# Performance work log

Measured on AMD Instinct MI355X. Metric: run time of the kernel, lower is better.

The kernel has to match this reference:

```python
import jax, jax.numpy as jnp
import numpy as np

B, S, L, K, E, V = 2048, 4, 16, 8, 256, 128  # batch, max_steps, tokens/step, landmarks/cell, emb_sz, vocab


def setup_inputs() -> dict:
    key = jax.random.key(0)
    ks = jax.random.split(key, 10)
    std = 1.0 / (E * 9)
    return {
        "gold_table": jax.random.normal(ks[0], (11, E), jnp.float32),
        "map_table": jax.random.normal(ks[1], (V, E), jnp.float32) * 0.01,  # init_std=0.01
        "conv_weight": jax.random.uniform(ks[2], (E, E, 3, 3), jnp.float32, -std, std),
        "action_table": jax.random.normal(ks[3], (4, 32), jnp.float32),
        "action_W": jax.random.normal(ks[4], (9, 32), jnp.float32) * (1.0 / np.sqrt(32.0)),
        "action_b": jnp.zeros((9,), jnp.float32),
        "goldstandard": jax.random.randint(ks[5], (B, S, L), 0, 11),
        "actions": jax.random.randint(ks[6], (B, S - 1), 0, 4),
        "landmarks": jax.random.randint(ks[7], (B, 4, 4, K), 0, V),
        "y": jax.random.randint(ks[8], (B, 2), 0, 4),
    }


def _extract_patches(x):
    # x: [B,E,4,4] -> [B,9,E,16]; 3x3 neighborhoods with zero padding (conv padding=1)
    xp = jnp.pad(x, ((0, 0), (0, 0), (1, 1), (1, 1)))
    shifts = [xp[:, :, dh:dh + 4, dw:dw + 4].reshape(x.shape[0], x.shape[1], 16)
              for dh in range(3) for dw in range(3)]
    return jnp.stack(shifts, axis=1)


def reference(gold_table, map_table, conv_weight, action_table, action_W, action_b,
              goldstandard, actions, landmarks, y):
    Bn = y.shape[0]
    # goldstandard features: per-step embed+sum over tokens, concat over steps -> [B, S*E]
    emb = gold_table[goldstandard].sum(axis=2).reshape(Bn, -1)
    # MapEmbedding2d with padding_idx=0: zero row 0, embed, sum over landmark list
    mt = map_table.at[0].set(0.0)
    l_emb = mt[landmarks].sum(axis=3).transpose(0, 3, 1, 2)  # [B,E,4,4]
    # action-conditioned 3x3 masks, one per action
    action_out = action_table @ action_W.T + action_b  # [4,9]
    masks = jax.nn.softmax(action_out, axis=1)  # [4,9]
    Wr = conv_weight.reshape(E, E, 9)  # [O,I,tap]
    l_embs = [l_emb]
    cur = l_emb
    for j in range(S - 1):
        # per-sample routed mask == dispatch-to-expert conv; fused gather+masked-conv+scatter
        m = masks[actions[:, j]]  # [B,9]
        patches = _extract_patches(cur)  # [B,9,E,16]
        out = jnp.einsum('btip,bt,oit->bop', patches, m, Wr).reshape(Bn, E, 4, 4)
        l_embs.append(out)
        cur = out
    lm = jnp.concatenate(l_embs, axis=1).reshape(Bn, S * E, 16)  # [B, S*E, 16]
    logits = jnp.einsum('bcp,bc->bp', lm, emb)  # bmm(landmarks^T, emb)
    prob = jax.nn.softmax(logits, axis=1)
    y_true = y[:, 0] * 4 + y[:, 1]
    # torch CrossEntropyLoss applied to prob (softmax twice, as in the original)
    logp = jax.nn.log_softmax(prob, axis=1)
    loss = -jnp.take_along_axis(logp, y_true[:, None], axis=1).mean()
    acc = (jnp.argmax(prob, axis=1) == y_true).astype(jnp.float32).mean()
    return loss, acc, prob
```

## Files before the change

kernel.cpp:

```cpp
#include <hip/hip_runtime.h>
#include <hip/hip_bf16.h>

typedef __attribute__((ext_vector_type(4))) float f32x4;
typedef __attribute__((ext_vector_type(8))) short short8;

__device__ __forceinline__ float bf2f(ushort u) {
    union { unsigned int u; float f; } x; x.u = ((unsigned int)u) << 16; return x.f;
}
__device__ __forceinline__ ushort f2bf(float f) {
    union { float f; unsigned int u; } x; x.f = f;
    unsigned int u = x.u;
    unsigned int r = (u + 0x7fffu + ((u >> 16) & 1u)) >> 16;
    return (ushort)r;
}
__device__ __forceinline__ void gload16(const ushort* g, ushort* l) {
    __builtin_amdgcn_global_load_lds(
        (const __attribute__((address_space(1))) unsigned int*)g,
        (__attribute__((address_space(3))) unsigned int*)l, 16, 0, 0);
}

__global__ __launch_bounds__(256) void k_prep(
    const float* __restrict__ conv_w, const float* __restrict__ a_table,
    const float* __restrict__ a_W, const float* __restrict__ a_b,
    const int* __restrict__ actions, int* __restrict__ cnt,
    int* __restrict__ list, ushort* __restrict__ Wa,
    float* __restrict__ out_head)
{
    __shared__ float ao[4][9];
    __shared__ float m[4][9];
    const int bid = blockIdx.x, tid = threadIdx.x;
    if (bid < 256) {
        if (tid < 36) {
            const int a = tid / 9, t = tid % 9;
            float s = a_b[t];
            for (int c = 0; c < 32; c++) s += a_table[a * 32 + c] * a_W[t * 32 + c];
            ao[a][t] = s;
        }
        __syncthreads();
        if (tid < 4) {
            float mx = -1e30f;
            for (int t = 0; t < 9; t++) mx = fmaxf(mx, ao[tid][t]);
            float e[9], z = 0.f;
            for (int t = 0; t < 9; t++) { e[t] = expf(ao[tid][t] - mx); z += e[t]; }
            for (int t = 0; t < 9; t++) m[tid][t] = e[t] / z;
        }
        __syncthreads();
        const int o = bid;
        float w9[9];
        #pragma unroll
        for (int t = 0; t < 9; t++) w9[t] = conv_w[(o * 256 + tid) * 9 + t];
        #pragma unroll
        for (int a = 0; a < 4; a++)
            #pragma unroll
            for (int t = 0; t < 9; t++)
                Wa[(size_t)((a << 8) + o) * 2304 + t * 256 + tid] = f2bf(m[a][t] * w9[t]);
    } else {
        if (tid < 12) cnt[tid] = 0;
        if (tid == 0) { out_head[0] = 0.f; out_head[1] = 0.f; }
        __syncthreads();
        for (int it = 0; it < 24; it++) {
            const int idx = it * 256 + tid;
            const int jj = idx >> 11, b = idx & 2047;
            const int av = actions[b * 3 + jj];
            const int pos = atomicAdd(&cnt[jj * 4 + av], 1);
            list[((jj * 4 + av) << 11) + pos] = b;
        }
    }
}

__global__ __launch_bounds__(256) void k_lemb(
    const float* __restrict__ mapt, const int* __restrict__ lms,
    ushort* __restrict__ c0)
{
    const int b = blockIdx.x, e = threadIdx.x;
    for (int p = 0; p < 16; p++) {
        const int* lm = lms + (b * 16 + p) * 8;
        float s = 0.f;
        #pragma unroll
        for (int k = 0; k < 8; k++) {
            const int idx = lm[k];
            if (idx) s += mapt[idx * 256 + e];
        }
        c0[(size_t)(b * 16 + p) * 256 + e] = f2bf(s);
    }
}

__global__ __launch_bounds__(256, 4) void k_conv(
    const ushort* __restrict__ cur, const ushort* __restrict__ Wa,
    const int* __restrict__ cnt, const int* __restrict__ list,
    const int j, ushort* __restrict__ outp)
{
    __shared__ __align__(16) ushort Alds[2][128 * 64];
    const int tid = threadIdx.x;

    const int c0n = cnt[j * 4 + 0], c1n = cnt[j * 4 + 1],
              c2n = cnt[j * 4 + 2], c3n = cnt[j * 4 + 3];
    const int t0 = (c0n + 3) >> 2;
    const int t1 = t0 + ((c1n + 3) >> 2);
    const int t2 = t1 + ((c2n + 3) >> 2);
    const int t3 = t2 + ((c3n + 3) >> 2);
    const int bid = blockIdx.x;
    const int wg2 = (bid & 7) * 129 + (bid >> 3);
    const int om  = wg2 >= 516 ? 1 : 0;
    const int g   = wg2 - om * 516;
    if (g >= t3) return;
    int a, off, ca;
    if      (g < t0) { a = 0; off = 0;  ca = c0n; }
    else if (g < t1) { a = 1; off = t0; ca = c1n; }
    else if (g < t2) { a = 2; off = t1; ca = c2n; }
    else             { a = 3; off = t2; ca = c3n; }
    const int slot0 = (g - off) * 4;
    const int* la = list + ((j * 4 + a) << 11);
    const ushort* wbase = Wa + (size_t)(a << 8) * 2304 + (size_t)om * 128 * 2304;

    const int wid = tid >> 6, lane = tid & 63;
    const int l15 = lane & 15, l4 = lane >> 4;
    const int wm = wid >> 1, wn = wid & 1;

    int sid[2]; bool vst[2];
    #pragma unroll
    for (int nf = 0; nf < 2; nf++) {
        const int sl = slot0 + wn * 2 + nf;
        vst[nf] = sl < ca;
        sid[nf] = vst[nf] ? la[sl] : 0;
    }

    const int srow = tid >> 3, sc = tid & 7;
    #define STAGE(buf, k0)                                                     \
        _Pragma("unroll")                                                      \
        for (int qq = 0; qq < 4; qq++) {                                       \
            const int row = qq * 32 + srow;                                    \
            const int cc = sc ^ (row & 7);                                     \
            gload16(wbase + (size_t)row * 2304 + (k0) + cc * 8,                \
                    &Alds[buf][qq * 2048 + tid * 8]);                          \
        }

    f32x4 acc[4][2];
    #pragma unroll
    for (int mf = 0; mf < 4; mf++) {
        acc[mf][0] = (f32x4){0.f, 0.f, 0.f, 0.f};
        acc[mf][1] = (f32x4){0.f, 0.f, 0.f, 0.f};
    }

    const short8 bzero = {0, 0, 0, 0, 0, 0, 0, 0};
    const int ph = l15 >> 2, pw = l15 & 3;

    short8 bcur[2][2], bnxt[2][2];
    #define LOADB(dst, ks)                                                     \
        {                                                                      \
            const int k0b = (ks) * 64;                                         \
            const int tb = k0b >> 8, i0b = k0b & 255;                          \
            const int hh = ph + tb / 3 - 1, ww = pw + tb % 3 - 1;              \
            const bool xv = (hh >= 0) & (hh < 4) & (ww >= 0) & (ww < 4);       \
            const int psrc = (hh << 2) + ww;                                   \
            _Pragma("unroll")                                                  \
            for (int nf = 0; nf < 2; nf++)                                     \
                _Pragma("unroll")                                              \
                for (int kf = 0; kf < 2; kf++) {                               \
                    const int i = i0b + kf * 32 + l4 * 8;                      \
                    const ushort* srcb =                                       \
                        cur + ((size_t)sid[nf] * 16 + psrc) * 256 + i;         \
                    dst[nf][kf] = xv ? *(const short8*)srcb : bzero;           \
                }                                                              \
        }

    LOADB(bcur, 0);
    STAGE(0, 0);

    int cb = 0;
    for (int ks = 0; ks < 36; ks++) {
        __syncthreads();
        if (ks + 1 < 36) STAGE(cb ^ 1, ks * 64 + 64);
        LOADB(bnxt, ks + 1);

        #pragma unroll
        for (int kf = 0; kf < 2; kf++)
            #pragma unroll
            for (int mf = 0; mf < 4; mf++) {
                const int rr = wm * 64 + mf * 16 + l15;
                const int cc = (kf * 4 + l4) ^ (rr & 7);
                const short8 af = *(const short8*)&Alds[cb][rr * 64 + cc * 8];
                acc[mf][0] = __builtin_amdgcn_mfma_f32_16x16x32_bf16(
                    af, bcur[0][kf], acc[mf][0], 0, 0, 0);
                acc[mf][1] = __builtin_amdgcn_mfma_f32_16x16x32_bf16(
                    af, bcur[1][kf], acc[mf][1], 0, 0, 0);
            }
        #pragma unroll
        for (int nf = 0; nf < 2; nf++)
            #pragma unroll
            for (int kf = 0; kf < 2; kf++) bcur[nf][kf] = bnxt[nf][kf];
        cb ^= 1;
    }

    #pragma unroll
    for (int nf = 0; nf < 2; nf++) {
        if (!vst[nf]) continue;
        const size_t rowb = ((size_t)sid[nf] * 16 + l15) * 256;
        #pragma unroll
        for (int mf = 0; mf < 4; mf++) {
            const int ob = om * 128 + wm * 64 + mf * 16 + l4 * 4;
            ushort o4[4];
            #pragma unroll
            for (int r = 0; r < 4; r++) o4[r] = f2bf(acc[mf][nf][r]);
            *(uint2*)&outp[rowb + ob] = *(const uint2*)o4;
        }
    }
    #undef STAGE
    #undef LOADB
}

__global__ __launch_bounds__(256) void k_final(
    const ushort* __restrict__ c0, const ushort* __restrict__ c1,
    const ushort* __restrict__ c2, const ushort* __restrict__ c3,
    const float* __restrict__ gold, const int* __restrict__ gs,
    const int* __restrict__ y, float* __restrict__ d_out)
{
    __shared__ float embl[4][256];
    __shared__ float red[256];
    __shared__ float lg[16];
    const int b = blockIdx.x, tid = threadIdx.x;
    {
        const int s = tid >> 6, e0 = (tid & 63) * 4;
        const int* g = gs + b * 64 + s * 16;
        float4 accv = make_float4(0.f, 0.f, 0.f, 0.f);
        #pragma unroll
        for (int l = 0; l < 16; l++) {
            const float4 v = *(const float4*)&gold[g[l] * 256 + e0];
            accv.x += v.x; accv.y += v.y; accv.z += v.z; accv.w += v.w;
        }
        *(float4*)&embl[s][e0] = accv;
    }
    __syncthreads();
    const int p = tid >> 4, g16 = tid & 15;
    const ushort* rows[4] = {
        c0 + (size_t)(b * 16 + p) * 256, c1 + (size_t)(b * 16 + p) * 256,
        c2 + (size_t)(b * 16 + p) * 256, c3 + (size_t)(b * 16 + p) * 256 };
    float acc = 0.f;
    #pragma unroll
    for (int s = 0; s < 4; s++) {
        const ushort* row = rows[s];
        const float* eb = embl[s];
        #pragma unroll 4
        for (int q = 0; q < 16; q++) {
            const int e = g16 + q * 16;
            acc += bf2f(row[e]) * eb[e];
        }
    }
    red[tid] = acc;
    __syncthreads();
    for (int st = 8; st >= 1; st >>= 1) {
        if (g16 < st) red[tid] += red[tid + st];
        __syncthreads();
    }
    if (g16 == 0) lg[p] = red[tid];
    __syncthreads();
    if (tid == 0) {
        float mx = -1e30f;
        for (int q = 0; q < 16; q++) mx = fmaxf(mx, lg[q]);
        float ex[16], z = 0.f;
        for (int q = 0; q < 16; q++) { ex[q] = expf(lg[q] - mx); z += ex[q]; }
        float prob[16];
        for (int q = 0; q < 16; q++) {
            prob[q] = ex[q] / z;
            d_out[2 + b * 16 + q] = prob[q];
        }
        int am = 0; float bv = prob[0];
        for (int q = 1; q < 16; q++) if (prob[q] > bv) { bv = prob[q]; am = q; }
        const int yt = y[b * 2] * 4 + y[b * 2 + 1];
        float z2 = 0.f;
        for (int q = 0; q < 16; q++) z2 += expf(prob[q]);
        const float logp = prob[yt] - logf(z2);
        atomicAdd(&d_out[0], -logp * (1.0f / 2048.0f));
        atomicAdd(&d_out[1], (am == yt) ? (1.0f / 2048.0f) : 0.0f);
    }
}

extern "C" void kernel_launch(void* const* d_in, const int* in_sizes, int n_in,
                              void* d_out, int out_size, void* d_ws, size_t ws_size,
                              hipStream_t stream) {
    const float* gold_table = (const float*)d_in[0];
    const float* map_table  = (const float*)d_in[1];
    const float* conv_w     = (const float*)d_in[2];
    const float* a_table    = (const float*)d_in[3];
    const float* a_W        = (const float*)d_in[4];
    const float* a_b        = (const float*)d_in[5];
    const int*   gs         = (const int*)d_in[6];
    const int*   actions    = (const int*)d_in[7];
    const int*   lms        = (const int*)d_in[8];
    const int*   y          = (const int*)d_in[9];
    float* out = (float*)d_out;

    char* ws = (char*)d_ws;
    int*    cnt  = (int*)(ws + 0);
    int*    list = (int*)(ws + 256);
    ushort* Wa   = (ushort*)(ws + 131072);
    ushort* c0   = (ushort*)(ws + 4849664);
    ushort* c1   = (ushort*)(ws + 21626880);
    ushort* c2   = (ushort*)(ws + 38404096);
    ushort* c3   = (ushort*)(ws + 55181312);
    (void)in_sizes; (void)n_in; (void)out_size; (void)ws_size;

    k_prep <<<257, 256, 0, stream>>>(conv_w, a_table, a_W, a_b, actions,
                                     cnt, list, Wa, out);
    k_lemb <<<2048, 256, 0, stream>>>(map_table, lms, c0);
    k_conv <<<1032, 256, 0, stream>>>(c0, Wa, cnt, list, 0, c1);
    k_conv <<<1032, 256, 0, stream>>>(c1, Wa, cnt, list, 1, c2);
    k_conv <<<1032, 256, 0, stream>>>(c2, Wa, cnt, list, 2, c3);
    k_final<<<2048, 256, 0, stream>>>(c0, c1, c2, c3, gold_table, gs, y, out);
}
```

Baseline: 483.5 us.

## Drop LDS staging in conv, widen sample tile, load A/B fragments directly

The conv kernel no longer stages weights through LDS with global_load_lds. Each wave now loads its A fragments straight from global memory into registers, with a two-deep software pipeline and no __syncthreads. Each block covers 8 samples instead of 4 (4x4 MFMA tiles per wave), which halves the grid and doubles reuse of each A fragment, at the cost of more registers (occupancy bound lowered to 2) and uncoalesced A loads served by cache. The final kernel also vectorises its bf16 row reads and pads its shared embedding buffer to avoid bank conflicts.

```diff
diff --git a/kernel.cpp b/kernel.cpp
--- a/kernel.cpp
+++ b/kernel.cpp
@@ -12,11 +12,6 @@
     unsigned int u = x.u;
     unsigned int r = (u + 0x7fffu + ((u >> 16) & 1u)) >> 16;
     return (ushort)r;
-}
-__device__ __forceinline__ void gload16(const ushort* g, ushort* l) {
-    __builtin_amdgcn_global_load_lds(
-        (const __attribute__((address_space(1))) unsigned int*)g,
-        (__attribute__((address_space(3))) unsigned int*)l, 16, 0, 0);
 }
 
 __global__ __launch_bounds__(256) void k_prep(
@@ -85,115 +80,96 @@
     }
 }
 
-__global__ __launch_bounds__(256, 4) void k_conv(
+__global__ __launch_bounds__(256, 2) void k_conv(
     const ushort* __restrict__ cur, const ushort* __restrict__ Wa,
     const int* __restrict__ cnt, const int* __restrict__ list,
     const int j, ushort* __restrict__ outp)
 {
-    __shared__ __align__(16) ushort Alds[2][128 * 64];
     const int tid = threadIdx.x;
 
     const int c0n = cnt[j * 4 + 0], c1n = cnt[j * 4 + 1],
               c2n = cnt[j * 4 + 2], c3n = cnt[j * 4 + 3];
-    const int t0 = (c0n + 3) >> 2;
-    const int t1 = t0 + ((c1n + 3) >> 2);
-    const int t2 = t1 + ((c2n + 3) >> 2);
-    const int t3 = t2 + ((c3n + 3) >> 2);
+    const int t0 = (c0n + 7) >> 3;
+    const int t1 = t0 + ((c1n + 7) >> 3);
+    const int t2 = t1 + ((c2n + 7) >> 3);
+    const int t3 = t2 + ((c3n + 7) >> 3);
     const int bid = blockIdx.x;
-    const int wg2 = (bid & 7) * 129 + (bid >> 3);
-    const int om  = wg2 >= 516 ? 1 : 0;
-    const int g   = wg2 - om * 516;
+    const int wg2 = (bid & 7) * 65 + (bid >> 3);
+    const int om  = wg2 >= 260 ? 1 : 0;
+    const int g   = wg2 - om * 260;
     if (g >= t3) return;
     int a, off, ca;
     if      (g < t0) { a = 0; off = 0;  ca = c0n; }
     else if (g < t1) { a = 1; off = t0; ca = c1n; }
     else if (g < t2) { a = 2; off = t1; ca = c2n; }
     else             { a = 3; off = t2; ca = c3n; }
-    const int slot0 = (g - off) * 4;
+    const int slot0 = (g - off) * 8;
     const int* la = list + ((j * 4 + a) << 11);
-    const ushort* wbase = Wa + (size_t)(a << 8) * 2304 + (size_t)om * 128 * 2304;
 
     const int wid = tid >> 6, lane = tid & 63;
     const int l15 = lane & 15, l4 = lane >> 4;
     const int wm = wid >> 1, wn = wid & 1;
 
-    int sid[2]; bool vst[2];
-    #pragma unroll
-    for (int nf = 0; nf < 2; nf++) {
-        const int sl = slot0 + wn * 2 + nf;
+    int sid[4]; bool vst[4];
+    #pragma unroll
+    for (int nf = 0; nf < 4; nf++) {
+        const int sl = slot0 + wn * 4 + nf;
         vst[nf] = sl < ca;
         sid[nf] = vst[nf] ? la[sl] : 0;
     }
 
-    const int srow = tid >> 3, sc = tid & 7;
-    #define STAGE(buf, k0)                                                     \
+    const ushort* abase =
+        Wa + (size_t)((a << 8) + om * 128 + wm * 64 + l15) * 2304 + l4 * 8;
+    const ushort* bs[4];
+    #pragma unroll
+    for (int nf = 0; nf < 4; nf++)
+        bs[nf] = cur + (size_t)sid[nf] * 4096 + l4 * 8;
+
+    const int ph = l15 >> 2, pw = l15 & 3;
+    const short8 bzero = {0, 0, 0, 0, 0, 0, 0, 0};
+
+    f32x4 acc[4][4];
+    #pragma unroll
+    for (int mf = 0; mf < 4; mf++)
+        #pragma unroll
+        for (int nf = 0; nf < 4; nf++) acc[mf][nf] = (f32x4){0.f, 0.f, 0.f, 0.f};
+
+    short8 A0[4], B0[4], A1[4], B1[4];
+
+    #define LOADA(d, ks)                                                       \
         _Pragma("unroll")                                                      \
-        for (int qq = 0; qq < 4; qq++) {                                       \
-            const int row = qq * 32 + srow;                                    \
-            const int cc = sc ^ (row & 7);                                     \
-            gload16(wbase + (size_t)row * 2304 + (k0) + cc * 8,                \
-                    &Alds[buf][qq * 2048 + tid * 8]);                          \
-        }
-
-    f32x4 acc[4][2];
-    #pragma unroll
-    for (int mf = 0; mf < 4; mf++) {
-        acc[mf][0] = (f32x4){0.f, 0.f, 0.f, 0.f};
-        acc[mf][1] = (f32x4){0.f, 0.f, 0.f, 0.f};
-    }
-
-    const short8 bzero = {0, 0, 0, 0, 0, 0, 0, 0};
-    const int ph = l15 >> 2, pw = l15 & 3;
-
-    short8 bcur[2][2], bnxt[2][2];
-    #define LOADB(dst, ks)                                                     \
+        for (int mf = 0; mf < 4; mf++)                                         \
+            d[mf] = *(const short8*)(abase + mf * 36864 + (ks) * 32);
+    #define LOADB(d, ks)                                                       \
         {                                                                      \
-            const int k0b = (ks) * 64;                                         \
-            const int tb = k0b >> 8, i0b = k0b & 255;                          \
-            const int hh = ph + tb / 3 - 1, ww = pw + tb % 3 - 1;              \
+            const int tn = (ks) >> 3, i0b = ((ks) & 7) * 32;                   \
+            const int td = (tn * 11) >> 5;                 \
+            const int tm = tn - 3 * td;                                        \
+            const int hh = ph + td - 1, ww = pw + tm - 1;                      \
             const bool xv = (hh >= 0) & (hh < 4) & (ww >= 0) & (ww < 4);       \
-            const int psrc = (hh << 2) + ww;                                   \
+            const int po = ((hh << 2) + ww) * 256 + i0b;                       \
             _Pragma("unroll")                                                  \
-            for (int nf = 0; nf < 2; nf++)                                     \
-                _Pragma("unroll")                                              \
-                for (int kf = 0; kf < 2; kf++) {                               \
-                    const int i = i0b + kf * 32 + l4 * 8;                      \
-                    const ushort* srcb =                                       \
-                        cur + ((size_t)sid[nf] * 16 + psrc) * 256 + i;         \
-                    dst[nf][kf] = xv ? *(const short8*)srcb : bzero;           \
-                }                                                              \
-        }
-
-    LOADB(bcur, 0);
-    STAGE(0, 0);
-
-    int cb = 0;
-    for (int ks = 0; ks < 36; ks++) {
-        __syncthreads();
-        if (ks + 1 < 36) STAGE(cb ^ 1, ks * 64 + 64);
-        LOADB(bnxt, ks + 1);
-
-        #pragma unroll
-        for (int kf = 0; kf < 2; kf++)
-            #pragma unroll
-            for (int mf = 0; mf < 4; mf++) {
-                const int rr = wm * 64 + mf * 16 + l15;
-                const int cc = (kf * 4 + l4) ^ (rr & 7);
-                const short8 af = *(const short8*)&Alds[cb][rr * 64 + cc * 8];
-                acc[mf][0] = __builtin_amdgcn_mfma_f32_16x16x32_bf16(
-                    af, bcur[0][kf], acc[mf][0], 0, 0, 0);
-                acc[mf][1] = __builtin_amdgcn_mfma_f32_16x16x32_bf16(
-                    af, bcur[1][kf], acc[mf][1], 0, 0, 0);
-            }
-        #pragma unroll
-        for (int nf = 0; nf < 2; nf++)
-            #pragma unroll
-            for (int kf = 0; kf < 2; kf++) bcur[nf][kf] = bnxt[nf][kf];
-        cb ^= 1;
-    }
-
-    #pragma unroll
-    for (int nf = 0; nf < 2; nf++) {
+            for (int nf = 0; nf < 4; nf++)                                     \
+                d[nf] = xv ? *(const short8*)(bs[nf] + po) : bzero;            \
+        }
+    #define MFMA16(Af, Bf)                                                     \
+        _Pragma("unroll")                                                      \
+        for (int mf = 0; mf < 4; mf++)                                         \
+            _Pragma("unroll")                                                  \
+            for (int nf = 0; nf < 4; nf++)                                     \
+                acc[mf][nf] = __builtin_amdgcn_mfma_f32_16x16x32_bf16(         \
+                    Af[mf], Bf[nf], acc[mf][nf], 0, 0, 0);
+
+    LOADA(A0, 0); LOADB(B0, 0);
+    for (int ks = 0; ks < 72; ks += 2) {
+        LOADA(A1, ks + 1); LOADB(B1, ks + 1);
+        MFMA16(A0, B0);
+        LOADA(A0, ks + 2); LOADB(B0, ks + 2);
+        MFMA16(A1, B1);
+    }
+
+    #pragma unroll
+    for (int nf = 0; nf < 4; nf++) {
         if (!vst[nf]) continue;
         const size_t rowb = ((size_t)sid[nf] * 16 + l15) * 256;
         #pragma unroll
@@ -205,8 +181,9 @@
             *(uint2*)&outp[rowb + ob] = *(const uint2*)o4;
         }
     }
-    #undef STAGE
+    #undef LOADA
     #undef LOADB
+    #undef MFMA16
 }
 
 __global__ __launch_bounds__(256) void k_final(
@@ -215,7 +192,7 @@
     const float* __restrict__ gold, const int* __restrict__ gs,
     const int* __restrict__ y, float* __restrict__ d_out)
 {
-    __shared__ float embl[4][256];
+    __shared__ float embl[4][272];
     __shared__ float red[256];
     __shared__ float lg[16];
     const int b = blockIdx.x, tid = threadIdx.x;
@@ -228,7 +205,8 @@
             const float4 v = *(const float4*)&gold[g[l] * 256 + e0];
             accv.x += v.x; accv.y += v.y; accv.z += v.z; accv.w += v.w;
         }
-        *(float4*)&embl[s][e0] = accv;
+        float* dst = &embl[s][(e0 >> 4) * 17 + (e0 & 15)];
+        dst[0] = accv.x; dst[1] = accv.y; dst[2] = accv.z; dst[3] = accv.w;
     }
     __syncthreads();
     const int p = tid >> 4, g16 = tid & 15;
@@ -238,13 +216,16 @@
     float acc = 0.f;
     #pragma unroll
     for (int s = 0; s < 4; s++) {
-        const ushort* row = rows[s];
-        const float* eb = embl[s];
-        #pragma unroll 4
-        for (int q = 0; q < 16; q++) {
-            const int e = g16 + q * 16;
-            acc += bf2f(row[e]) * eb[e];
-        }
+        const ushort* row = rows[s] + g16 * 16;
+        const uint4 v0 = *(const uint4*)row;
+        const uint4 v1 = *(const uint4*)(row + 8);
+        const ushort* pv0 = (const ushort*)&v0;
+        const ushort* pv1 = (const ushort*)&v1;
+        const float* eb = &embl[s][g16 * 17];
+        #pragma unroll
+        for (int q = 0; q < 8; q++) acc += bf2f(pv0[q]) * eb[q];
+        #pragma unroll
+        for (int q = 0; q < 8; q++) acc += bf2f(pv1[q]) * eb[8 + q];
     }
     red[tid] = acc;
     __syncthreads();
@@ -303,8 +284,8 @@
     k_prep <<<257, 256, 0, stream>>>(conv_w, a_table, a_W, a_b, actions,
                                      cnt, list, Wa, out);
     k_lemb <<<2048, 256, 0, stream>>>(map_table, lms, c0);
-    k_conv <<<1032, 256, 0, stream>>>(c0, Wa, cnt, list, 0, c1);
-    k_conv <<<1032, 256, 0, stream>>>(c1, Wa, cnt, list, 1, c2);
-    k_conv <<<1032, 256, 0, stream>>>(c2, Wa, cnt, list, 2, c3);
+    k_conv <<<520, 256, 0, stream>>>(c0, Wa, cnt, list, 0, c1);
+    k_conv <<<520, 256, 0, stream>>>(c1, Wa, cnt, list, 1, c2);
+    k_conv <<<520, 256, 0, stream>>>(c2, Wa, cnt, list, 2, c3);
     k_final<<<2048, 256, 0, stream>>>(c0, c1, c2, c3, gold_table, gs, y, out);
 }
```

Result: slower. 710.7 us (+47.0%).
